# Kernel optimization log

Measured on AMD Instinct MI355X. Metric: run time of the kernel, lower is better.

Reference implementation:

```python
import jax, jax.numpy as jnp
import numpy as np

NUM_HEADS = 8
LN_EPS = 1e-5


def _pos_enc(h, w, dim, dtype):
    # PositionalEncodingPermute2D: channels = ceil(dim/2)
    ch = int(np.ceil(dim / 2))
    inv = jnp.asarray(1.0 / (10000.0 ** (np.arange(0, ch, 2, dtype=np.float32) / ch)))
    px = jnp.arange(h, dtype=jnp.float32)[:, None] * inv  # (h, ch//2)
    py = jnp.arange(w, dtype=jnp.float32)[:, None] * inv  # (w, ch//2)
    ex = jnp.concatenate([jnp.sin(px), jnp.cos(px)], -1)  # (h, ch)
    ey = jnp.concatenate([jnp.sin(py), jnp.cos(py)], -1)  # (w, ch)
    emb = jnp.concatenate([
        jnp.broadcast_to(ex[:, None, :], (h, w, ch)),
        jnp.broadcast_to(ey[None, :, :], (h, w, ch)),
    ], -1)[:, :, :dim]  # (h, w, dim)
    return emb.transpose(2, 0, 1).astype(dtype)  # (dim, h, w)


def _pool(x, s):
    # AdaptiveAvgPool2d(s) with h, w divisible by s
    b, c, h, w = x.shape
    return x.reshape(b, c, s, h // s, s, w // s).mean((3, 5))


def _dsc(y, dw_w, pw_w):
    # depthwise 3x3 (groups=C, pad 1, no bias) + pointwise 1x1 (no bias)
    dn = ('NCHW', 'OIHW', 'NCHW')
    y = jax.lax.conv_general_dilated(y, dw_w, (1, 1), 'SAME',
                                     feature_group_count=y.shape[1],
                                     dimension_numbers=dn)
    return jax.lax.conv_general_dilated(y, pw_w, (1, 1), 'SAME',
                                        dimension_numbers=dn)


def setup_inputs() -> dict:
    key = jax.random.key(0)
    ks = jax.random.split(key, 8)
    b, c, h, w = 8, 128, 128, 128
    s = 0.02
    return {
        'x': jax.random.normal(ks[0], (b, c, h, w), jnp.float32),
        'Wq': jax.random.normal(ks[1], (c, c), jnp.float32) * s,
        'Wkv': jax.random.normal(ks[2], (2 * c, c), jnp.float32) * s,
        'Wproj': jax.random.normal(ks[3], (c, c), jnp.float32) * s,
        'bproj': jnp.zeros((c,), jnp.float32),
        'dw_w': jax.random.normal(ks[4], (c, 1, 3, 3), jnp.float32) * np.sqrt(2.0 / 9.0),
        'pw_w': jax.random.normal(ks[5], (c, c, 1, 1), jnp.float32) * np.sqrt(2.0 / c),
        'ln_w': jnp.ones((c,), jnp.float32),
        'ln_b': jnp.zeros((c,), jnp.float32),
    }


def reference(x, Wq, Wkv, Wproj, bproj, dw_w, pw_w, ln_w, ln_b):
    b, c, h, w = x.shape
    m = NUM_HEADS
    hd = c // m
    scale = hd ** -0.5

    xp = x + _pos_enc(h, w, c, x.dtype)[None]        # (b,c,h,w)
    xt = xp.reshape(b, c, h * w).transpose(0, 2, 1)  # (b,hw,c)

    q = (xt @ Wq.T).reshape(b, h * w, m, hd).transpose(0, 2, 1, 3)  # (b,m,hw,hd)

    # four ASPP branches through the shared depthwise-separable conv
    branches = []
    for s in (8, 4, 2, 1):
        y = _dsc(_pool(xp, s), dw_w, pw_w)           # (b,c,s,s)
        branches.append(y.reshape(b, c, s * s).transpose(0, 2, 1))
    z = jnp.concatenate(branches, axis=1)            # (b,85,c)

    mu = z.mean(-1, keepdims=True)
    var = ((z - mu) ** 2).mean(-1, keepdims=True)
    z = (z - mu) / jnp.sqrt(var + LN_EPS) * ln_w + ln_b
    z = jax.nn.gelu(z, approximate=False)

    kvlen = z.shape[1]
    kv = (z @ Wkv.T).reshape(b, kvlen, 2, m, hd).transpose(2, 0, 3, 1, 4)  # (2,b,m,kv,hd)
    k, v = kv[0], kv[1]

    attn = jax.nn.softmax(jnp.einsum('bmqd,bmkd->bmqk', q, k) * scale, axis=-1)
    o = jnp.einsum('bmqk,bmkd->bmqd', attn, v)       # (b,m,hw,hd)
    o = o.transpose(0, 2, 1, 3).reshape(b, h * w, c)
    o = o @ Wproj.T + bproj                          # dropout p=0 (eval) is identity
    return o.transpose(0, 2, 1).reshape(b, c, h, w)
```

## Files before the change

kernel.cpp:

```cpp
#include <hip/hip_runtime.h>
#include <stdint.h>

#define OFF_XT   ((size_t)0)
#define OFF_EX   ((size_t)33554432)
#define OFF_EY   (OFF_EX + 32768)
#define OFF_WQB  (OFF_EY + 32768)
#define OFF_WPB  (OFF_WQB + 32768)
#define OFF_P8   (OFF_WPB + 32768)
#define OFF_KWS  (OFF_P8 + 262144)
#define OFF_VWS  (OFF_KWS + 196608)

typedef __attribute__((ext_vector_type(4)))  float f32x4;
typedef __attribute__((ext_vector_type(16))) float f32x16;
typedef __attribute__((ext_vector_type(8)))  short s16x8;

__device__ __forceinline__ uint16_t f2bf(float f){
  uint32_t u = __builtin_bit_cast(uint32_t, f);
  u += 0x7fffu + ((u >> 16) & 1u);
  return (uint16_t)(u >> 16);
}
__device__ __forceinline__ float bf2f(uint16_t h){
  uint32_t u = ((uint32_t)h) << 16;
  return __builtin_bit_cast(float, u);
}

__global__ __launch_bounds__(256) void kprep(const float* __restrict__ Wq,
                                             const float* __restrict__ Wproj,
                                             char* __restrict__ ws){
  int idx = blockIdx.x * 256 + threadIdx.x;
  float* EX = (float*)(ws + OFF_EX);
  float* EY = (float*)(ws + OFF_EY);
  uint16_t* WQB = (uint16_t*)(ws + OFF_WQB);
  uint16_t* WPB = (uint16_t*)(ws + OFF_WPB);
  if (idx < 8192){
    int i = idx >> 6, d = idx & 63;
    int k = d & 31;
    float inv = powf(10000.0f, -(float)k * (1.0f/32.0f));
    float a = (float)i * inv;
    EX[idx] = (d < 32) ? sinf(a) : cosf(a);
  } else if (idx < 16384){
    int e = idx - 8192;
    int c = e >> 7, j = e & 127;
    int k = c & 31;
    float inv = powf(10000.0f, -(float)k * (1.0f/32.0f));
    float a = (float)j * inv;
    EY[e] = (c < 32) ? sinf(a) : cosf(a);
  } else if (idx < 32768){
    int e = idx - 16384;
    WQB[e] = f2bf(Wq[e]);
  } else if (idx < 49152){
    int e = idx - 32768;
    WPB[e] = f2bf(Wproj[e]);
  }
}

__global__ __launch_bounds__(256) void ktrans(const float* __restrict__ x,
                                              char* __restrict__ ws){
  const float* EX = (const float*)(ws + OFF_EX);
  const float* EY = (const float*)(ws + OFF_EY);
  uint16_t* XT = (uint16_t*)(ws + OFF_XT);
  int t = threadIdx.x;
  int bx = blockIdx.x;
  int b  = bx >> 9;
  int ct = (bx >> 8) & 1;
  int pt = bx & 255;
  int c0 = ct * 64;
  int pix0 = pt * 64;
  int i  = pix0 >> 7;
  int j0 = pix0 & 127;

  __shared__ float tile[64][65];
  int pix = t & 63;
  int cl  = t >> 6;
  #pragma unroll
  for (int it = 0; it < 16; ++it){
    int c = it*4 + cl;
    int cg = c0 + c;
    float v = x[((size_t)(b*128 + cg))*16384 + pix0 + pix];
    v += (cg < 64) ? EX[i*64 + cg] : EY[(cg-64)*128 + j0 + pix];
    tile[c][pix] = v;
  }
  __syncthreads();
  int g  = t & 15;
  int pr = t >> 4;
  #pragma unroll
  for (int it = 0; it < 4; ++it){
    int p2 = it*16 + pr;
    ushort4 o;
    o.x = f2bf(tile[g*4+0][p2]);
    o.y = f2bf(tile[g*4+1][p2]);
    o.z = f2bf(tile[g*4+2][p2]);
    o.w = f2bf(tile[g*4+3][p2]);
    *(ushort4*)(XT + ((size_t)(b*16384) + pix0 + p2)*128 + c0 + g*4) = o;
  }
}

__global__ __launch_bounds__(256) void kpool(char* __restrict__ ws){
  const uint16_t* XT = (const uint16_t*)(ws + OFF_XT);
  float* P8 = (float*)(ws + OFF_P8);
  int t = threadIdx.x;
  int bx = blockIdx.x;
  int b = bx >> 6;
  int bin = bx & 63;
  int bi = bin >> 3, bj = bin & 7;
  int c = t & 127, half = t >> 7;
  float acc = 0.f;
  for (int r = 0; r < 8; ++r){
    int irow = bi*16 + half*8 + r;
    const uint16_t* row = XT + ((size_t)(b*16384) + irow*128 + bj*16)*128 + c;
    #pragma unroll
    for (int jj = 0; jj < 16; ++jj)
      acc += bf2f(row[jj*128]);
  }
  __shared__ float red[256];
  red[t] = acc;
  __syncthreads();
  if (t < 128){
    float s = red[t] + red[t+128];
    P8[((size_t)(b*128) + c)*64 + bin] = s * (1.0f/256.0f);
  }
}

__global__ __launch_bounds__(256) void kaspp(const float* __restrict__ dww,
                                             const float* __restrict__ pww,
                                             const float* __restrict__ Wkv,
                                             const float* __restrict__ lnw,
                                             const float* __restrict__ lnb,
                                             char* __restrict__ ws){
  const float* P8 = (const float*)(ws + OFF_P8);
  uint16_t* KWS = (uint16_t*)(ws + OFF_KWS);
  uint16_t* VWS = (uint16_t*)(ws + OFF_VWS);
  int bx = blockIdx.x;
  int b = bx / 96;
  int pos = bx % 96;
  int t = threadIdx.x;

  if (pos >= 85){
    if (t < 128){
      int m = t >> 4, hd = t & 15;
      KWS[(((size_t)b*8 + m)*96 + pos)*16 + hd] = 0;
      VWS[(((size_t)b*8 + m)*16 + hd)*96 + pos] = 0;
    }
    return;
  }

  int s, si, sj;
  if (pos < 64){ s = 8; si = pos >> 3; sj = pos & 7; }
  else if (pos < 80){ int e = pos - 64; s = 4; si = e >> 2; sj = e & 3; }
  else if (pos < 84){ int e = pos - 80; s = 2; si = e >> 1; sj = e & 1; }
  else { s = 1; si = 0; sj = 0; }

  __shared__ float yl[128], zl[128], red[128], red2[128];

  if (t < 128){
    int c = t;
    int bs = 8 / s;
    float y = 0.f;
    const float* p8 = P8 + ((size_t)(b*128) + c)*64;
    float binv = 1.0f / (float)(bs*bs);
    for (int di = -1; di <= 1; ++di)
      for (int dj = -1; dj <= 1; ++dj){
        int a = si + di, bb = sj + dj;
        if (a >= 0 && a < s && bb >= 0 && bb < s){
          float pv = 0.f;
          for (int u = 0; u < bs; ++u)
            for (int v = 0; v < bs; ++v)
              pv += p8[(a*bs + u)*8 + (bb*bs + v)];
          y += pv * binv * dww[c*9 + (di+1)*3 + (dj+1)];
        }
      }
    yl[t] = y;
  }
  __syncthreads();

  float acc = 0.f;
  if (t < 128){
    const float* wr = pww + (size_t)t*128;
    for (int cin = 0; cin < 128; ++cin) acc += wr[cin] * yl[cin];
    red[t] = acc; red2[t] = acc*acc;
  }
  __syncthreads();
  for (int off = 64; off >= 1; off >>= 1){
    if (t < off){ red[t] += red[t+off]; red2[t] += red2[t+off]; }
    __syncthreads();
  }
  float mu  = red[0] * (1.0f/128.0f);
  float var = red2[0] * (1.0f/128.0f) - mu*mu;
  if (t < 128){
    float z = (acc - mu) * rsqrtf(var + 1e-5f) * lnw[t] + lnb[t];
    float g = 0.5f * z * (1.0f + erff(z * 0.70710678118654752f));
    zl[t] = g;
  }
  __syncthreads();

  {
    float a2 = 0.f;
    const float* wr = Wkv + (size_t)t*128;
    for (int c2 = 0; c2 < 128; ++c2) a2 += wr[c2] * zl[c2];
    uint16_t bv = f2bf(a2);
    if (t < 128){
      int m = t >> 4, hd = t & 15;
      KWS[(((size_t)b*8 + m)*96 + pos)*16 + hd] = bv;
    } else {
      int tt = t - 128;
      int m = tt >> 4, hd = tt & 15;
      VWS[(((size_t)b*8 + m)*16 + hd)*96 + pos] = bv;
    }
  }
}

__global__ __launch_bounds__(256) void kmain(const char* __restrict__ wsc,
                                             const float* __restrict__ bproj,
                                             float* __restrict__ out){
  const char* ws = wsc;
  const uint16_t* XT  = (const uint16_t*)(ws + OFF_XT);
  const uint16_t* WQB = (const uint16_t*)(ws + OFF_WQB);
  const uint16_t* WPB = (const uint16_t*)(ws + OFF_WPB);
  const uint16_t* KWS = (const uint16_t*)(ws + OFF_KWS);
  const uint16_t* VWS = (const uint16_t*)(ws + OFF_VWS);

  __shared__ __align__(16) char smem[65536];
  const int t = threadIdx.x;
  const int lane = t & 63;
  const int wv = t >> 6;
  const int bx = blockIdx.x;
  const int b = bx >> 8;
  const int pix0 = (bx & 255) * 64;

  {
    const uint16_t* src = XT + ((size_t)(b*16384 + pix0))*128;
    #pragma unroll
    for (int pass = 0; pass < 4; ++pass){
      int pix = pass*16 + (t >> 4);
      int g = t & 15;
      uint4 v = *(const uint4*)(src + (size_t)pix*128 + g*8);
      int dst = pix*256 + ((g*16) ^ ((pix & 7) << 4));
      *(uint4*)(smem + dst) = v;
    }
  }
  __syncthreads();

  {
    s16x8 afr[4];
    int pixl = wv*16 + (lane & 15);
    #pragma unroll
    for (int ks = 0; ks < 4; ++ks){
      int kb = ks*32 + 8*(lane >> 4);
      afr[ks] = *(const s16x8*)(smem + pixl*256 + ((kb*2) ^ ((pixl & 7) << 4)));
    }
    #pragma unroll
    for (int nt = 0; nt < 8; ++nt){
      int nq = nt*16 + (lane & 15);
      f32x4 acc = {0.f, 0.f, 0.f, 0.f};
      #pragma unroll
      for (int ks = 0; ks < 4; ++ks){
        s16x8 bfr = *(const s16x8*)(WQB + nq*128 + ks*32 + 8*(lane >> 4));
        acc = __builtin_amdgcn_mfma_f32_16x16x32_bf16(afr[ks], bfr, acc, 0, 0, 0);
      }
      #pragma unroll
      for (int r = 0; r < 4; ++r){
        int pix = wv*16 + 4*(lane >> 4) + r;
        *(uint16_t*)(smem + 32768 + pix*256 + ((nq*2) ^ ((pix & 7) << 4))) = f2bf(acc[r]);
      }
    }
  }
  __syncthreads();

  {
    const int ph = wv & 1;
    const int h0 = (wv >> 1) * 4;
    char* Pw = smem + wv*8192;
    const int hi = lane >> 5;
    const float C1 = 0.36067376022224085f;

    #pragma unroll 1
    for (int h = h0; h < h0 + 4; ++h){
      int pixq = ph*32 + (lane & 31);
      int kbq = h*16 + 8*(lane >> 5);
      s16x8 qf = *(const s16x8*)(smem + 32768 + pixq*256 + ((kbq*2) ^ ((pixq & 7) << 4)));

      f32x16 sa[3];
      #pragma unroll
      for (int mt = 0; mt < 3; ++mt){
        int kv = mt*32 + (lane & 31);
        s16x8 kf = *(const s16x8*)(KWS + (((size_t)(b*8 + h))*96 + kv)*16 + 8*(lane >> 5));
        f32x16 z;
        #pragma unroll
        for (int r2 = 0; r2 < 16; ++r2) z[r2] = 0.f;
        sa[mt] = __builtin_amdgcn_mfma_f32_32x32x16_bf16(kf, qf, z, 0, 0, 0);
      }
      float mx = -3.0e38f;
      #pragma unroll
      for (int mt = 0; mt < 3; ++mt)
        #pragma unroll
        for (int r = 0; r < 16; ++r){
          int kv = mt*32 + (r & 3) + 8*(r >> 2) + 4*hi;
          if (kv < 85) mx = fmaxf(mx, sa[mt][r]);
        }
      mx = fmaxf(mx, __shfl_xor(mx, 32));
      float sum = 0.f;
      #pragma unroll
      for (int mt = 0; mt < 3; ++mt)
        #pragma unroll
        for (int r = 0; r < 16; ++r){
          int kv = mt*32 + (r & 3) + 8*(r >> 2) + 4*hi;
          float p = (kv < 85) ? exp2f((sa[mt][r] - mx) * C1) : 0.f;
          sa[mt][r] = p;
          sum += p;
        }
      sum += __shfl_xor(sum, 32);
      float rinv = 1.0f / sum;

      int pixp = lane & 31;
      #pragma unroll
      for (int mt = 0; mt < 3; ++mt)
        #pragma unroll
        for (int rp = 0; rp < 8; ++rp){
          int r = rp*2;
          int kv = mt*32 + (r & 3) + 8*(r >> 2) + 4*hi;
          uint32_t pk = (uint32_t)f2bf(sa[mt][r] * rinv)
                      | ((uint32_t)f2bf(sa[mt][r+1] * rinv) << 16);
          *(uint32_t*)(Pw + pixp*256 + ((kv*2) ^ ((pixp & 7) << 4))) = pk;
        }

      #pragma unroll
      for (int nt2 = 0; nt2 < 2; ++nt2){
        f32x4 oacc = {0.f, 0.f, 0.f, 0.f};
        int hd = lane & 15;
        int pixv = nt2*16 + (lane & 15);
        #pragma unroll
        for (int ksv = 0; ksv < 3; ++ksv){
          int kvb = ksv*32 + 8*(lane >> 4);
          s16x8 vf = *(const s16x8*)(VWS + (((size_t)(b*8 + h))*16 + hd)*96 + kvb);
          s16x8 pf = *(const s16x8*)(Pw + pixv*256 + ((kvb*2) ^ ((pixv & 7) << 4)));
          oacc = __builtin_amdgcn_mfma_f32_16x16x32_bf16(vf, pf, oacc, 0, 0, 0);
        }
        int pixb = ph*32 + nt2*16 + (lane & 15);
        #pragma unroll
        for (int rp = 0; rp < 2; ++rp){
          int cidx = h*16 + 4*(lane >> 4) + rp*2;
          uint32_t pk = (uint32_t)f2bf(oacc[rp*2])
                      | ((uint32_t)f2bf(oacc[rp*2+1]) << 16);
          *(uint32_t*)(smem + 49152 + pixb*256 + ((cidx*2) ^ ((pixb & 7) << 4))) = pk;
        }
      }
    }
  }
  __syncthreads();

  {
    s16x8 ofr[4];
    int pix = wv*16 + (lane & 15);
    #pragma unroll
    for (int ks = 0; ks < 4; ++ks){
      int kb = ks*32 + 8*(lane >> 4);
      ofr[ks] = *(const s16x8*)(smem + 49152 + pix*256 + ((kb*2) ^ ((pix & 7) << 4)));
    }
    int pixg = pix0 + pix;
    #pragma unroll 1
    for (int mtc = 0; mtc < 8; ++mtc){
      int coutb = mtc*16 + (lane & 15);
      f32x4 acc = {0.f, 0.f, 0.f, 0.f};
      #pragma unroll
      for (int ks = 0; ks < 4; ++ks){
        s16x8 af = *(const s16x8*)(WPB + coutb*128 + ks*32 + 8*(lane >> 4));
        acc = __builtin_amdgcn_mfma_f32_16x16x32_bf16(af, ofr[ks], acc, 0, 0, 0);
      }
      f32x4 bias = *(const f32x4*)(bproj + mtc*16 + 4*(lane >> 4));
      #pragma unroll
      for (int r = 0; r < 4; ++r){
        int cout = mtc*16 + 4*(lane >> 4) + r;
        out[((size_t)(b*128 + cout))*16384 + pixg] = acc[r] + bias[r];
      }
    }
  }
}

extern "C" void kernel_launch(void* const* d_in, const int* in_sizes, int n_in,
                              void* d_out, int out_size, void* d_ws, size_t ws_size,
                              hipStream_t stream){
  const float* x     = (const float*)d_in[0];
  const float* Wq    = (const float*)d_in[1];
  const float* Wkv   = (const float*)d_in[2];
  const float* Wproj = (const float*)d_in[3];
  const float* bproj = (const float*)d_in[4];
  const float* dww   = (const float*)d_in[5];
  const float* pww   = (const float*)d_in[6];
  const float* lnw   = (const float*)d_in[7];
  const float* lnb   = (const float*)d_in[8];
  char* ws = (char*)d_ws;
  float* out = (float*)d_out;

  kprep<<<192, 256, 0, stream>>>(Wq, Wproj, ws);
  ktrans<<<4096, 256, 0, stream>>>(x, ws);
  kpool<<<512, 256, 0, stream>>>(ws);
  kaspp<<<768, 256, 0, stream>>>(dww, pww, Wkv, lnw, lnb, ws);
  kmain<<<2048, 256, 0, stream>>>(ws, bproj, out);
}
```

Before: 257.6 us.

## Fuse transpose into attention kernel, pool raw x directly, keep P in registers

```diff
diff --git a/kernel.cpp b/kernel.cpp
--- a/kernel.cpp
+++ b/kernel.cpp
@@ -1,27 +1,30 @@
 #include <hip/hip_runtime.h>
 #include <stdint.h>
 
-#define OFF_XT   ((size_t)0)
-#define OFF_EX   ((size_t)33554432)
-#define OFF_EY   (OFF_EX + 32768)
-#define OFF_WQB  (OFF_EY + 32768)
-#define OFF_WPB  (OFF_WQB + 32768)
-#define OFF_P8   (OFF_WPB + 32768)
-#define OFF_KWS  (OFF_P8 + 262144)
-#define OFF_VWS  (OFF_KWS + 196608)
+#define OFF_EX   ((size_t)0)
+#define OFF_EY   ((size_t)32768)
+#define OFF_EXM  ((size_t)65536)
+#define OFF_EYM  ((size_t)67584)
+#define OFF_WQB  ((size_t)69632)
+#define OFF_WPB  ((size_t)102400)
+#define OFF_P8   ((size_t)135168)
+#define OFF_KWS  ((size_t)393216)
+#define OFF_VWS  ((size_t)589824)
 
 typedef __attribute__((ext_vector_type(4)))  float f32x4;
 typedef __attribute__((ext_vector_type(16))) float f32x16;
 typedef __attribute__((ext_vector_type(8)))  short s16x8;
+typedef __attribute__((ext_vector_type(4)))  unsigned int u32x4;
 
 __device__ __forceinline__ uint16_t f2bf(float f){
   uint32_t u = __builtin_bit_cast(uint32_t, f);
   u += 0x7fffu + ((u >> 16) & 1u);
   return (uint16_t)(u >> 16);
 }
-__device__ __forceinline__ float bf2f(uint16_t h){
-  uint32_t u = ((uint32_t)h) << 16;
-  return __builtin_bit_cast(float, u);
+__device__ __forceinline__ uint32_t cvtpk(float a, float b){
+  uint32_t r;
+  asm("v_cvt_pk_bf16_f32 %0, %1, %2" : "=v"(r) : "v"(a), "v"(b));
+  return r;
 }
 
 __global__ __launch_bounds__(256) void kprep(const float* __restrict__ Wq,
@@ -30,19 +33,19 @@
   int idx = blockIdx.x * 256 + threadIdx.x;
   float* EX = (float*)(ws + OFF_EX);
   float* EY = (float*)(ws + OFF_EY);
+  float* EXM = (float*)(ws + OFF_EXM);
+  float* EYM = (float*)(ws + OFF_EYM);
   uint16_t* WQB = (uint16_t*)(ws + OFF_WQB);
   uint16_t* WPB = (uint16_t*)(ws + OFF_WPB);
   if (idx < 8192){
     int i = idx >> 6, d = idx & 63;
-    int k = d & 31;
-    float inv = powf(10000.0f, -(float)k * (1.0f/32.0f));
+    float inv = powf(10000.0f, -(float)(d & 31) * (1.0f/32.0f));
     float a = (float)i * inv;
     EX[idx] = (d < 32) ? sinf(a) : cosf(a);
   } else if (idx < 16384){
     int e = idx - 8192;
     int c = e >> 7, j = e & 127;
-    int k = c & 31;
-    float inv = powf(10000.0f, -(float)k * (1.0f/32.0f));
+    float inv = powf(10000.0f, -(float)(c & 31) * (1.0f/32.0f));
     float a = (float)j * inv;
     EY[e] = (c < 32) ? sinf(a) : cosf(a);
   } else if (idx < 32768){
@@ -51,73 +54,56 @@
   } else if (idx < 49152){
     int e = idx - 32768;
     WPB[e] = f2bf(Wproj[e]);
-  }
-}
-
-__global__ __launch_bounds__(256) void ktrans(const float* __restrict__ x,
+  } else if (idx < 49664){
+    int e = idx - 49152; int r8 = e >> 6, c = e & 63;
+    float inv = powf(10000.0f, -(float)(c & 31) * (1.0f/32.0f));
+    float s = 0.f;
+    for (int u = 0; u < 16; ++u){
+      float a = (float)(r8*16 + u) * inv;
+      s += (c < 32) ? sinf(a) : cosf(a);
+    }
+    EXM[e] = s * (1.0f/16.0f);
+  } else if (idx < 50176){
+    int e = idx - 49664; int c8 = e >> 6, c2 = e & 63;
+    float inv = powf(10000.0f, -(float)(c2 & 31) * (1.0f/32.0f));
+    float s = 0.f;
+    for (int w = 0; w < 16; ++w){
+      float a = (float)(c8*16 + w) * inv;
+      s += (c2 < 32) ? sinf(a) : cosf(a);
+    }
+    EYM[e] = s * (1.0f/16.0f);
+  }
+}
+
+__global__ __launch_bounds__(256) void kpool2(const float* __restrict__ x,
                                               char* __restrict__ ws){
-  const float* EX = (const float*)(ws + OFF_EX);
-  const float* EY = (const float*)(ws + OFF_EY);
-  uint16_t* XT = (uint16_t*)(ws + OFF_XT);
-  int t = threadIdx.x;
+  float* P8 = (float*)(ws + OFF_P8);
   int bx = blockIdx.x;
-  int b  = bx >> 9;
-  int ct = (bx >> 8) & 1;
-  int pt = bx & 255;
-  int c0 = ct * 64;
-  int pix0 = pt * 64;
-  int i  = pix0 >> 7;
-  int j0 = pix0 & 127;
-
-  __shared__ float tile[64][65];
-  int pix = t & 63;
-  int cl  = t >> 6;
+  int b = bx >> 7, c = bx & 127;
+  int t = threadIdx.x, lane = t & 63, wv = t >> 6;
+  const float* plane = x + ((size_t)(b*128 + c))*16384;
+  float acc[8];
   #pragma unroll
-  for (int it = 0; it < 16; ++it){
-    int c = it*4 + cl;
-    int cg = c0 + c;
-    float v = x[((size_t)(b*128 + cg))*16384 + pix0 + pix];
-    v += (cg < 64) ? EX[i*64 + cg] : EY[(cg-64)*128 + j0 + pix];
-    tile[c][pix] = v;
-  }
-  __syncthreads();
-  int g  = t & 15;
-  int pr = t >> 4;
+  for (int r = 0; r < 8; ++r) acc[r] = 0.f;
   #pragma unroll
-  for (int it = 0; it < 4; ++it){
-    int p2 = it*16 + pr;
-    ushort4 o;
-    o.x = f2bf(tile[g*4+0][p2]);
-    o.y = f2bf(tile[g*4+1][p2]);
-    o.z = f2bf(tile[g*4+2][p2]);
-    o.w = f2bf(tile[g*4+3][p2]);
-    *(ushort4*)(XT + ((size_t)(b*16384) + pix0 + p2)*128 + c0 + g*4) = o;
-  }
-}
-
-__global__ __launch_bounds__(256) void kpool(char* __restrict__ ws){
-  const uint16_t* XT = (const uint16_t*)(ws + OFF_XT);
-  float* P8 = (float*)(ws + OFF_P8);
-  int t = threadIdx.x;
-  int bx = blockIdx.x;
-  int b = bx >> 6;
-  int bin = bx & 63;
-  int bi = bin >> 3, bj = bin & 7;
-  int c = t & 127, half = t >> 7;
-  float acc = 0.f;
-  for (int r = 0; r < 8; ++r){
-    int irow = bi*16 + half*8 + r;
-    const uint16_t* row = XT + ((size_t)(b*16384) + irow*128 + bj*16)*128 + c;
-    #pragma unroll
-    for (int jj = 0; jj < 16; ++jj)
-      acc += bf2f(row[jj*128]);
-  }
-  __shared__ float red[256];
-  red[t] = acc;
-  __syncthreads();
-  if (t < 128){
-    float s = red[t] + red[t+128];
-    P8[((size_t)(b*128) + c)*64 + bin] = s * (1.0f/256.0f);
+  for (int k = 0; k < 16; ++k){
+    f32x4 v = *(const f32x4*)(plane + k*1024 + t*4);
+    acc[k >> 1] += (v.x + v.y) + (v.z + v.w);
+  }
+  __shared__ float wred[4][64];
+  int bc = (lane >> 2) & 7;
+  #pragma unroll
+  for (int br = 0; br < 8; ++br){
+    float v = acc[br];
+    v += __shfl_xor(v, 1);
+    v += __shfl_xor(v, 2);
+    v += __shfl_xor(v, 32);
+    if ((lane & 3) == 0 && lane < 32) wred[wv][br*8 + bc] = v;
+  }
+  __syncthreads();
+  if (t < 64){
+    float s = wred[0][t] + wred[1][t] + wred[2][t] + wred[3][t];
+    P8[((size_t)(b*128) + c)*64 + t] = s * (1.0f/256.0f);
   }
 }
 
@@ -127,7 +113,9 @@
                                              const float* __restrict__ lnw,
                                              const float* __restrict__ lnb,
                                              char* __restrict__ ws){
-  const float* P8 = (const float*)(ws + OFF_P8);
+  const float* P8  = (const float*)(ws + OFF_P8);
+  const float* EXM = (const float*)(ws + OFF_EXM);
+  const float* EYM = (const float*)(ws + OFF_EYM);
   uint16_t* KWS = (uint16_t*)(ws + OFF_KWS);
   uint16_t* VWS = (uint16_t*)(ws + OFF_VWS);
   int bx = blockIdx.x;
@@ -152,6 +140,7 @@
 
   __shared__ float yl[128], zl[128], red[128], red2[128];
 
+  float acc = 0.f;
   if (t < 128){
     int c = t;
     int bs = 8 / s;
@@ -164,8 +153,11 @@
         if (a >= 0 && a < s && bb >= 0 && bb < s){
           float pv = 0.f;
           for (int u = 0; u < bs; ++u)
-            for (int v = 0; v < bs; ++v)
-              pv += p8[(a*bs + u)*8 + (bb*bs + v)];
+            for (int v = 0; v < bs; ++v){
+              int r8 = a*bs + u, c8 = bb*bs + v;
+              float pe = (c < 64) ? EXM[r8*64 + c] : EYM[c8*64 + (c - 64)];
+              pv += p8[r8*8 + c8] + pe;
+            }
           y += pv * binv * dww[c*9 + (di+1)*3 + (dj+1)];
         }
       }
@@ -173,7 +165,6 @@
   }
   __syncthreads();
 
-  float acc = 0.f;
   if (t < 128){
     const float* wr = pww + (size_t)t*128;
     for (int cin = 0; cin < 128; ++cin) acc += wr[cin] * yl[cin];
@@ -209,59 +200,85 @@
   }
 }
 
-__global__ __launch_bounds__(256) void kmain(const char* __restrict__ wsc,
-                                             const float* __restrict__ bproj,
-                                             float* __restrict__ out){
+__global__ __launch_bounds__(256, 3) void kmain(const char* __restrict__ wsc,
+                                                const float* __restrict__ x,
+                                                const float* __restrict__ bproj,
+                                                float* __restrict__ out){
   const char* ws = wsc;
-  const uint16_t* XT  = (const uint16_t*)(ws + OFF_XT);
   const uint16_t* WQB = (const uint16_t*)(ws + OFF_WQB);
   const uint16_t* WPB = (const uint16_t*)(ws + OFF_WPB);
   const uint16_t* KWS = (const uint16_t*)(ws + OFF_KWS);
   const uint16_t* VWS = (const uint16_t*)(ws + OFF_VWS);
-
-  __shared__ __align__(16) char smem[65536];
+  const float* EX = (const float*)(ws + OFF_EX);
+  const float* EY = (const float*)(ws + OFF_EY);
+
+  __shared__ __align__(16) char smem[49152];
   const int t = threadIdx.x;
   const int lane = t & 63;
   const int wv = t >> 6;
   const int bx = blockIdx.x;
   const int b = bx >> 8;
   const int pix0 = (bx & 255) * 64;
-
-  {
-    const uint16_t* src = XT + ((size_t)(b*16384 + pix0))*128;
-    #pragma unroll
-    for (int pass = 0; pass < 4; ++pass){
-      int pix = pass*16 + (t >> 4);
-      int g = t & 15;
-      uint4 v = *(const uint4*)(src + (size_t)pix*128 + g*8);
-      int dst = pix*256 + ((g*16) ^ ((pix & 7) << 4));
-      *(uint4*)(smem + dst) = v;
-    }
-  }
-  __syncthreads();
-
-  {
-    s16x8 afr[4];
+  const int i  = pix0 >> 7;
+  const int j0 = pix0 & 127;
+
+  {
+    int csub = lane >> 4;
+    int p4 = (lane & 15) * 4;
+    #pragma unroll
+    for (int it = 0; it < 8; ++it){
+      int c = wv*32 + it*4 + csub;
+      f32x4 v = *(const f32x4*)(x + ((size_t)(b*128 + c))*16384 + pix0 + p4);
+      if (c < 64){
+        float pe = EX[i*64 + c];
+        v.x += pe; v.y += pe; v.z += pe; v.w += pe;
+      } else {
+        f32x4 pe = *(const f32x4*)(EY + (c - 64)*128 + j0 + p4);
+        v.x += pe.x; v.y += pe.y; v.z += pe.z; v.w += pe.w;
+      }
+      *(f32x4*)(smem + c*256 + p4*4) = v;
+    }
+  }
+  __syncthreads();
+
+  {
+    const float* tmp = (const float*)smem;
+    int pix = lane;
+    float f[32];
+    #pragma unroll
+    for (int j = 0; j < 32; ++j) f[j] = tmp[(wv*32 + j)*64 + pix];
+    uint32_t u[16];
+    #pragma unroll
+    for (int j = 0; j < 16; ++j) u[j] = cvtpk(f[2*j], f[2*j+1]);
+    #pragma unroll
+    for (int g = 0; g < 4; ++g){
+      u32x4 w4 = { u[g*4+0], u[g*4+1], u[g*4+2], u[g*4+3] };
+      int c0 = wv*32 + g*8;
+      *(u32x4*)(smem + 32768 + pix*256 + ((c0*2) ^ ((pix & 7) << 4))) = w4;
+    }
+  }
+  __syncthreads();
+
+  {
     int pixl = wv*16 + (lane & 15);
-    #pragma unroll
-    for (int ks = 0; ks < 4; ++ks){
-      int kb = ks*32 + 8*(lane >> 4);
-      afr[ks] = *(const s16x8*)(smem + pixl*256 + ((kb*2) ^ ((pixl & 7) << 4)));
-    }
+    s16x8 xfr[4];
+    #pragma unroll
+    for (int ks = 0; ks < 4; ++ks)
+      xfr[ks] = *(const s16x8*)(smem + 32768 + pixl*256 +
+                 ((ks*64 + (lane >> 4)*16) ^ ((pixl & 7) << 4)));
     #pragma unroll
     for (int nt = 0; nt < 8; ++nt){
-      int nq = nt*16 + (lane & 15);
       f32x4 acc = {0.f, 0.f, 0.f, 0.f};
       #pragma unroll
       for (int ks = 0; ks < 4; ++ks){
-        s16x8 bfr = *(const s16x8*)(WQB + nq*128 + ks*32 + 8*(lane >> 4));
-        acc = __builtin_amdgcn_mfma_f32_16x16x32_bf16(afr[ks], bfr, acc, 0, 0, 0);
-      }
-      #pragma unroll
-      for (int r = 0; r < 4; ++r){
-        int pix = wv*16 + 4*(lane >> 4) + r;
-        *(uint16_t*)(smem + 32768 + pix*256 + ((nq*2) ^ ((pix & 7) << 4))) = f2bf(acc[r]);
-      }
+        s16x8 wfr = *(const s16x8*)(WQB + (nt*16 + (lane & 15))*128 + ks*32 + 8*(lane >> 4));
+        acc = __builtin_amdgcn_mfma_f32_16x16x32_bf16(wfr, xfr[ks], acc, 0, 0, 0);
+      }
+      int nq0 = nt*16 + 4*(lane >> 4);
+      uint32_t w0 = cvtpk(acc[0], acc[1]);
+      uint32_t w1 = cvtpk(acc[2], acc[3]);
+      *(uint32_t*)(smem + pixl*256 + ((nq0*2) ^ ((pixl & 7) << 4))) = w0;
+      *(uint32_t*)(smem + pixl*256 + (((nq0 + 2)*2) ^ ((pixl & 7) << 4))) = w1;
     }
   }
   __syncthreads();
@@ -269,108 +286,108 @@
   {
     const int ph = wv & 1;
     const int h0 = (wv >> 1) * 4;
-    char* Pw = smem + wv*8192;
     const int hi = lane >> 5;
+    const int pixq = ph*32 + (lane & 31);
     const float C1 = 0.36067376022224085f;
 
     #pragma unroll 1
     for (int h = h0; h < h0 + 4; ++h){
-      int pixq = ph*32 + (lane & 31);
-      int kbq = h*16 + 8*(lane >> 5);
-      s16x8 qf = *(const s16x8*)(smem + 32768 + pixq*256 + ((kbq*2) ^ ((pixq & 7) << 4)));
-
+      const uint16_t* Kh = KWS + ((size_t)(b*8 + h))*1536;
+      const uint16_t* Vh = VWS + ((size_t)(b*8 + h))*1536;
+      s16x8 kf[3], vf[6];
+      #pragma unroll
+      for (int mt = 0; mt < 3; ++mt)
+        kf[mt] = *(const s16x8*)(Kh + (mt*32 + (lane & 31))*16 + 8*hi);
+      #pragma unroll
+      for (int kc = 0; kc < 6; ++kc)
+        vf[kc] = *(const s16x8*)(Vh + (lane & 15)*96 + kc*16 + 8*hi);
+      s16x8 qf = *(const s16x8*)(smem + pixq*256 + ((h*32 + hi*16) ^ ((pixq & 7) << 4)));
+
+      f32x16 zz;
+      #pragma unroll
+      for (int r = 0; r < 16; ++r) zz[r] = 0.f;
       f32x16 sa[3];
       #pragma unroll
-      for (int mt = 0; mt < 3; ++mt){
-        int kv = mt*32 + (lane & 31);
-        s16x8 kf = *(const s16x8*)(KWS + (((size_t)(b*8 + h))*96 + kv)*16 + 8*(lane >> 5));
-        f32x16 z;
-        #pragma unroll
-        for (int r2 = 0; r2 < 16; ++r2) z[r2] = 0.f;
-        sa[mt] = __builtin_amdgcn_mfma_f32_32x32x16_bf16(kf, qf, z, 0, 0, 0);
-      }
-      float mx = -3.0e38f;
-      #pragma unroll
       for (int mt = 0; mt < 3; ++mt)
-        #pragma unroll
-        for (int r = 0; r < 16; ++r){
-          int kv = mt*32 + (r & 3) + 8*(r >> 2) + 4*hi;
-          if (kv < 85) mx = fmaxf(mx, sa[mt][r]);
-        }
+        sa[mt] = __builtin_amdgcn_mfma_f32_32x32x16_bf16(kf[mt], qf, zz, 0, 0, 0);
+
+      float mx = 0.f;
+      #pragma unroll
+      for (int r = 0; r < 16; ++r){
+        mx = fmaxf(mx, sa[0][r]);
+        mx = fmaxf(mx, sa[1][r]);
+        mx = fmaxf(mx, sa[2][r]);
+      }
       mx = fmaxf(mx, __shfl_xor(mx, 32));
       float sum = 0.f;
       #pragma unroll
-      for (int mt = 0; mt < 3; ++mt)
-        #pragma unroll
-        for (int r = 0; r < 16; ++r){
-          int kv = mt*32 + (r & 3) + 8*(r >> 2) + 4*hi;
-          float p = (kv < 85) ? exp2f((sa[mt][r] - mx) * C1) : 0.f;
-          sa[mt][r] = p;
-          sum += p;
-        }
+      for (int r = 0; r < 16; ++r){
+        float p0 = exp2f((sa[0][r] - mx)*C1); sa[0][r] = p0; sum += p0;
+        float p1 = exp2f((sa[1][r] - mx)*C1); sa[1][r] = p1; sum += p1;
+        int kvb = (r & 3) + 8*(r >> 2) + 4*hi;
+        float p2 = (64 + kvb < 85) ? exp2f((sa[2][r] - mx)*C1) : 0.f;
+        sa[2][r] = p2; sum += p2;
+      }
       sum += __shfl_xor(sum, 32);
       float rinv = 1.0f / sum;
 
-      int pixp = lane & 31;
-      #pragma unroll
-      for (int mt = 0; mt < 3; ++mt)
+      f32x16 oacc = zz;
+      #pragma unroll
+      for (int mt = 0; mt < 3; ++mt){
+        uint32_t u0[4], u1[4];
         #pragma unroll
-        for (int rp = 0; rp < 8; ++rp){
-          int r = rp*2;
-          int kv = mt*32 + (r & 3) + 8*(r >> 2) + 4*hi;
-          uint32_t pk = (uint32_t)f2bf(sa[mt][r] * rinv)
-                      | ((uint32_t)f2bf(sa[mt][r+1] * rinv) << 16);
-          *(uint32_t*)(Pw + pixp*256 + ((kv*2) ^ ((pixp & 7) << 4))) = pk;
+        for (int q = 0; q < 4; ++q){
+          u0[q] = cvtpk(sa[mt][4*q + 0], sa[mt][4*q + 1]);
+          u1[q] = cvtpk(sa[mt][4*q + 2], sa[mt][4*q + 3]);
         }
-
-      #pragma unroll
-      for (int nt2 = 0; nt2 < 2; ++nt2){
-        f32x4 oacc = {0.f, 0.f, 0.f, 0.f};
-        int hd = lane & 15;
-        int pixv = nt2*16 + (lane & 15);
         #pragma unroll
-        for (int ksv = 0; ksv < 3; ++ksv){
-          int kvb = ksv*32 + 8*(lane >> 4);
-          s16x8 vf = *(const s16x8*)(VWS + (((size_t)(b*8 + h))*16 + hd)*96 + kvb);
-          s16x8 pf = *(const s16x8*)(Pw + pixv*256 + ((kvb*2) ^ ((pixv & 7) << 4)));
-          oacc = __builtin_amdgcn_mfma_f32_16x16x32_bf16(vf, pf, oacc, 0, 0, 0);
+        for (int c2 = 0; c2 < 2; ++c2){
+          uint32_t s0 = hi ? u0[2*c2] : u0[2*c2 + 1];
+          uint32_t s1 = hi ? u1[2*c2] : u1[2*c2 + 1];
+          uint32_t r0 = (uint32_t)__shfl_xor((int)s0, 32);
+          uint32_t r1 = (uint32_t)__shfl_xor((int)s1, 32);
+          u32x4 w4;
+          w4.x = hi ? r0 : u0[2*c2];
+          w4.y = hi ? r1 : u1[2*c2];
+          w4.z = hi ? u0[2*c2 + 1] : r0;
+          w4.w = hi ? u1[2*c2 + 1] : r1;
+          oacc = __builtin_amdgcn_mfma_f32_32x32x16_bf16(
+                   vf[mt*2 + c2], __builtin_bit_cast(s16x8, w4), oacc, 0, 0, 0);
         }
-        int pixb = ph*32 + nt2*16 + (lane & 15);
-        #pragma unroll
-        for (int rp = 0; rp < 2; ++rp){
-          int cidx = h*16 + 4*(lane >> 4) + rp*2;
-          uint32_t pk = (uint32_t)f2bf(oacc[rp*2])
-                      | ((uint32_t)f2bf(oacc[rp*2+1]) << 16);
-          *(uint32_t*)(smem + 49152 + pixb*256 + ((cidx*2) ^ ((pixb & 7) << 4))) = pk;
-        }
-      }
-    }
-  }
-  __syncthreads();
-
-  {
+      }
+      #pragma unroll
+      for (int p = 0; p < 4; ++p){
+        int hd0 = 4*hi + (p & 1)*2 + 8*(p >> 1);
+        uint32_t uo = cvtpk(oacc[2*p]*rinv, oacc[2*p + 1]*rinv);
+        int c0 = h*16 + hd0;
+        *(uint32_t*)(smem + 16384 + pixq*256 + ((c0*2) ^ ((pixq & 7) << 4))) = uo;
+      }
+    }
+  }
+  __syncthreads();
+
+  {
+    int pixl = wv*16 + (lane & 15);
     s16x8 ofr[4];
-    int pix = wv*16 + (lane & 15);
-    #pragma unroll
-    for (int ks = 0; ks < 4; ++ks){
-      int kb = ks*32 + 8*(lane >> 4);
-      ofr[ks] = *(const s16x8*)(smem + 49152 + pix*256 + ((kb*2) ^ ((pix & 7) << 4)));
-    }
-    int pixg = pix0 + pix;
-    #pragma unroll 1
+    #pragma unroll
+    for (int ks = 0; ks < 4; ++ks)
+      ofr[ks] = *(const s16x8*)(smem + 16384 + pixl*256 +
+                 ((ks*64 + (lane >> 4)*16) ^ ((pixl & 7) << 4)));
+    int pixg = pix0 + pixl;
+    float* outb = out + (size_t)b*128*16384 + pixg;
+    #pragma unroll 2
     for (int mtc = 0; mtc < 8; ++mtc){
-      int coutb = mtc*16 + (lane & 15);
       f32x4 acc = {0.f, 0.f, 0.f, 0.f};
       #pragma unroll
       for (int ks = 0; ks < 4; ++ks){
-        s16x8 af = *(const s16x8*)(WPB + coutb*128 + ks*32 + 8*(lane >> 4));
-        acc = __builtin_amdgcn_mfma_f32_16x16x32_bf16(af, ofr[ks], acc, 0, 0, 0);
+        s16x8 wf = *(const s16x8*)(WPB + (mtc*16 + (lane & 15))*128 + ks*32 + 8*(lane >> 4));
+        acc = __builtin_amdgcn_mfma_f32_16x16x32_bf16(wf, ofr[ks], acc, 0, 0, 0);
       }
       f32x4 bias = *(const f32x4*)(bproj + mtc*16 + 4*(lane >> 4));
       #pragma unroll
       for (int r = 0; r < 4; ++r){
         int cout = mtc*16 + 4*(lane >> 4) + r;
-        out[((size_t)(b*128 + cout))*16384 + pixg] = acc[r] + bias[r];
+        outb[(size_t)cout*16384] = acc[r] + bias[r];
       }
     }
   }
@@ -391,9 +408,8 @@
   char* ws = (char*)d_ws;
   float* out = (float*)d_out;
 
-  kprep<<<192, 256, 0, stream>>>(Wq, Wproj, ws);
-  ktrans<<<4096, 256, 0, stream>>>(x, ws);
-  kpool<<<512, 256, 0, stream>>>(ws);
+  kprep<<<196, 256, 0, stream>>>(Wq, Wproj, ws);
+  kpool2<<<1024, 256, 0, stream>>>(x, ws);
   kaspp<<<768, 256, 0, stream>>>(dww, pww, Wkv, lnw, lnb, ws);
-  kmain<<<2048, 256, 0, stream>>>(ws, bproj, out);
-}
+  kmain<<<2048, 256, 0, stream>>>(ws, x, bproj, out);
+}
```

Result: faster. 242.4 us (-5.9%).
